# Performance work log

Measured on AMD Instinct MI355X. Metric: run time of the kernel, lower is better.

The kernel has to match this reference:

```python
import jax, jax.numpy as jnp
import numpy as np

N_NODES = 10000
N_EDGES = 640000
D_IN = 128
D_OUT = 128


def setup_inputs() -> dict:
    key = jax.random.key(0)
    ks = jax.random.split(key, 8)
    x = jax.random.normal(ks[0], (N_NODES, D_IN), dtype=jnp.float32)
    edge_index = jax.random.randint(ks[1], (2, N_EDGES), 0, N_NODES, dtype=jnp.int64)
    batch = jnp.zeros((N_NODES,), dtype=jnp.int64)
    s_in = 1.0 / np.sqrt(D_IN)
    s_out = 1.0 / np.sqrt(D_OUT)
    W_lin = jax.random.uniform(ks[2], (D_OUT, D_IN), jnp.float32, -s_in, s_in)
    b_lin = jax.random.uniform(ks[3], (D_OUT,), jnp.float32, -s_in, s_in)
    W_gate = jax.random.uniform(ks[4], (1, D_IN), jnp.float32, -s_in, s_in)
    b_gate = jax.random.uniform(ks[5], (1,), jnp.float32, -s_in, s_in)
    W_out = jax.random.uniform(ks[6], (D_OUT, D_OUT), jnp.float32, -s_out, s_out)
    b_out = jax.random.uniform(ks[7], (D_OUT,), jnp.float32, -s_out, s_out)
    return {"x": x, "edge_index": edge_index, "batch": batch,
            "W_lin": W_lin, "b_lin": b_lin, "W_gate": W_gate, "b_gate": b_gate,
            "W_out": W_out, "b_out": b_out}


def reference(x, edge_index, batch, W_lin, b_lin, W_gate, b_gate, W_out, b_out):
    row, col = edge_index[0], edge_index[1]
    n = x.shape[0]
    messages = x[col]                                      # [E, D_IN] gather
    gate = messages @ W_gate.T + b_gate                    # [E, 1]
    h = messages @ W_lin.T + b_lin                         # [E, D_OUT]
    # segment softmax over edges grouped by destination node (row)
    g = gate[:, 0]
    seg_max = jax.ops.segment_max(g, row, num_segments=n)  # -inf for empty segments (never gathered)
    e = jnp.exp(g - seg_max[row])
    denom = jax.ops.segment_sum(e, row, num_segments=n) + 1e-16
    attn = (e / denom[row])[:, None]                       # [E, 1]
    pooled = jax.ops.segment_sum(attn * h, row, num_segments=n)  # [N, D_OUT]
    return pooled @ W_out.T + b_out
```

## Files before the change

kernel.cpp:

```cpp
#include <hip/hip_runtime.h>
#include <math.h>

#define N_NODES_C 10000
#define N_EDGES_C 640000
#define DIM 128
#define NB 625
#define CAP 1344
#define CHUNK 4096
#define KPT 16
#define GATE_BLOCKS 2500
#define WC_BLOCKS 64
#define SCAT_BLOCKS ((N_EDGES_C + CHUNK - 1) / CHUNK)

__device__ __forceinline__ unsigned pack_bf16x2(float a, float b) {
    unsigned ua = __float_as_uint(a);
    unsigned ub = __float_as_uint(b);
    ua = (ua + 0x7FFFu + ((ua >> 16) & 1u)) >> 16;
    ub = (ub + 0x7FFFu + ((ub >> 16) & 1u)) >> 16;
    return ua | (ub << 16);
}
#define BF_LO(u) __uint_as_float((u) << 16)
#define BF_HI(u) __uint_as_float((u) & 0xFFFF0000u)

__global__ void prep_scatter_kernel(const float* __restrict__ x,
                                    const float* __restrict__ w_gate,
                                    const float* __restrict__ b_gate,
                                    const float* __restrict__ W_out,
                                    const float* __restrict__ W_lin,
                                    const float* __restrict__ b_lin,
                                    const int* __restrict__ row,
                                    const int* __restrict__ col,
                                    float* __restrict__ eg,
                                    unsigned* __restrict__ xh,
                                    int* __restrict__ bucket_fill,
                                    int* __restrict__ edata_b,
                                    float* __restrict__ WcT,
                                    float* __restrict__ bc,
                                    int n, int nE) {
    __shared__ int   histS[NB];
    __shared__ int   lbaseS[NB];
    __shared__ float wrow[2][DIM];
    __shared__ float red[2][DIM];
    int tid = threadIdx.x;
    int bx  = blockIdx.x;

    if (bx < SCAT_BLOCKS) {
        int sb = bx;
        for (int i = tid; i < NB; i += 256) histS[i] = 0;
        __syncthreads();

        int start = sb * CHUNK;
        int bkt[KPT], rnk[KPT], cl[KPT];
        #pragma unroll
        for (int k = 0; k < KPT; k++) {
            int e = start + k * 256 + tid;
            if (e < nE) {
                int r = row[e];
                int b = r >> 4;
                bkt[k] = b;
                cl[k]  = ((r & 15) << 16) | col[e];
                rnk[k] = atomicAdd(&histS[b], 1);
            } else { bkt[k] = -1; rnk[k] = 0; cl[k] = 0; }
        }
        __syncthreads();
        for (int i = tid; i < NB; i += 256)
            lbaseS[i] = histS[i] ? atomicAdd(&bucket_fill[i], histS[i]) : 0;
        __syncthreads();
        #pragma unroll
        for (int k = 0; k < KPT; k++) {
            if (bkt[k] >= 0) {
                int p = lbaseS[bkt[k]] + rnk[k];
                if (p < CAP)
                    edata_b[(size_t)bkt[k] * CAP + p] = cl[k];
            }
        }
    } else if (bx < SCAT_BLOCKS + WC_BLOCKS) {
        int grp = tid >> 7;
        int i   = tid & 127;
        int o   = (bx - SCAT_BLOCKS) * 2 + grp;
        wrow[grp][i] = W_out[o * DIM + i];
        __syncthreads();
        float acc = 0.f;
        #pragma unroll 8
        for (int k = 0; k < DIM; k++) acc += wrow[grp][k] * W_lin[k * DIM + i];
        WcT[i * DIM + o] = acc;
        red[grp][i] = wrow[grp][i] * b_lin[i];
        __syncthreads();
        for (int off = 64; off; off >>= 1) {
            if (i < off) red[grp][i] += red[grp][i + off];
            __syncthreads();
        }
        if (i == 0) bc[o] = red[grp][0];
    } else {
        int gid  = (bx - SCAT_BLOCKS - WC_BLOCKS) * 256 + tid;
        int wid  = gid >> 6;
        int lane = tid & 63;
        if (wid < n) {
            const float2* xr = (const float2*)(x + (size_t)wid * DIM);
            float2 a = xr[lane];
            float2 b = ((const float2*)w_gate)[lane];
            xh[(size_t)wid * 64 + lane] = pack_bf16x2(a.x, a.y);
            float v = a.x * b.x + a.y * b.y;
            #pragma unroll
            for (int off = 32; off; off >>= 1) v += __shfl_xor(v, off);
            if (lane == 0) eg[wid] = expf(v + b_gate[0]);
        }
    }
}

__global__ __launch_bounds__(512)
void bagg_kernel(const unsigned* __restrict__ xh,
                 const float* __restrict__ eg,
                 const int* __restrict__ edata_b,
                 const int* __restrict__ bucket_fill,
                 const float* __restrict__ WcT,
                 const float* __restrict__ bc,
                 const float* __restrict__ b_out,
                 float* __restrict__ out, int n) {
    __shared__ float aggT[16 * DIM];
    __shared__ float egS[N_NODES_C];
    __shared__ int  cntS[16], baseS[16], curS[16];
    __shared__ float sS[16];
    int* srt = (int*)aggT;

    int b   = blockIdx.x;
    int tid = threadIdx.x;
    int cnt = bucket_fill[b]; if (cnt > CAP) cnt = CAP;
    const int* eb = edata_b + (size_t)b * CAP;

    {
        const float4* eg4 = (const float4*)eg;
        float4* egS4 = (float4*)egS;
        #pragma unroll
        for (int k = 0; k < 5; k++) {
            int i = tid + k * 512;
            if (i < N_NODES_C / 4) egS4[i] = eg4[i];
        }
    }
    if (tid < 16) cntS[tid] = 0;
    __syncthreads();

    int rec[3];
    #pragma unroll
    for (int k = 0; k < 3; k++) {
        int j = tid + k * 512;
        rec[k] = (j < cnt) ? eb[j] : -1;
        if (rec[k] >= 0) atomicAdd(&cntS[rec[k] >> 16], 1);
    }
    __syncthreads();

    if (tid < 16) {
        int v = cntS[tid];
        int s = v;
        #pragma unroll
        for (int off = 1; off < 16; off <<= 1) {
            int t = __shfl_up(s, off);
            if (tid >= off) s += t;
        }
        baseS[tid] = s - v;
        curS[tid]  = s - v;
    }
    __syncthreads();

    #pragma unroll
    for (int k = 0; k < 3; k++) {
        if (rec[k] >= 0) {
            int p = atomicAdd(&curS[rec[k] >> 16], 1);
            srt[p] = rec[k] & 0xFFFF;
        }
    }
    __syncthreads();

    int l   = tid >> 5;
    int q   = (tid >> 4) & 1;
    int s16 = tid & 15;
    int beg = baseS[l];
    int end = beg + cntS[l];

    float a0=0.f,a1=0.f,a2=0.f,a3=0.f,a4=0.f,a5=0.f,a6=0.f,a7=0.f;
    float dl = 0.f;
    int j = beg;
    for (; j + 8 <= end; j += 8) {
        #pragma unroll
        for (int p = 0; p < 4; p++) {
            int   cc = srt[j + 2 * p + q];
            float e  = egS[cc];
            uint4 u  = ((const uint4*)(xh + (size_t)cc * 64))[s16];
            dl += e;
            a0 += e * BF_LO(u.x); a1 += e * BF_HI(u.x);
            a2 += e * BF_LO(u.y); a3 += e * BF_HI(u.y);
            a4 += e * BF_LO(u.z); a5 += e * BF_HI(u.z);
            a6 += e * BF_LO(u.w); a7 += e * BF_HI(u.w);
        }
    }
    for (; j + 2 <= end; j += 2) {
        int   cc = srt[j + q];
        float e  = egS[cc];
        uint4 u  = ((const uint4*)(xh + (size_t)cc * 64))[s16];
        dl += e;
        a0 += e * BF_LO(u.x); a1 += e * BF_HI(u.x);
        a2 += e * BF_LO(u.y); a3 += e * BF_HI(u.y);
        a4 += e * BF_LO(u.z); a5 += e * BF_HI(u.z);
        a6 += e * BF_LO(u.w); a7 += e * BF_HI(u.w);
    }
    if (j < end) {
        int   cc = srt[j];
        float e  = q ? 0.f : egS[cc];
        uint4 u  = ((const uint4*)(xh + (size_t)cc * 64))[s16];
        dl += e;
        a0 += e * BF_LO(u.x); a1 += e * BF_HI(u.x);
        a2 += e * BF_LO(u.y); a3 += e * BF_HI(u.y);
        a4 += e * BF_LO(u.z); a5 += e * BF_HI(u.z);
        a6 += e * BF_LO(u.w); a7 += e * BF_HI(u.w);
    }

    a0 += __shfl_xor(a0, 16); a1 += __shfl_xor(a1, 16);
    a2 += __shfl_xor(a2, 16); a3 += __shfl_xor(a3, 16);
    a4 += __shfl_xor(a4, 16); a5 += __shfl_xor(a5, 16);
    a6 += __shfl_xor(a6, 16); a7 += __shfl_xor(a7, 16);
    dl += __shfl_xor(dl, 16);
    float denom = dl;
    float inv   = 1.f / (denom + 1e-16f);

    __syncthreads();
    if (q == 0) {
        float4* dst = (float4*)(aggT + l * DIM + 8 * s16);
        dst[0] = make_float4(a0 * inv, a1 * inv, a2 * inv, a3 * inv);
        dst[1] = make_float4(a4 * inv, a5 * inv, a6 * inv, a7 * inv);
        if (s16 == 0) sS[l] = denom * inv;
    }
    __syncthreads();

    int grp = tid >> 7;
    int o   = tid & 127;
    int l0  = grp * 4;
    float bcv = bc[o];
    float bov = b_out[o];
    float o0 = 0.f, o1 = 0.f, o2 = 0.f, o3 = 0.f;
    const float* t0 = aggT + (l0 + 0) * DIM;
    const float* t1 = aggT + (l0 + 1) * DIM;
    const float* t2 = aggT + (l0 + 2) * DIM;
    const float* t3 = aggT + (l0 + 3) * DIM;
    #pragma unroll 4
    for (int i = 0; i < DIM; i++) {
        float w = WcT[i * DIM + o];
        o0 += w * t0[i];
        o1 += w * t1[i];
        o2 += w * t2[i];
        o3 += w * t3[i];
    }
    int nodeBase = (b << 4) + l0;
    if (nodeBase + 0 < n) out[(size_t)(nodeBase + 0) * DIM + o] = o0 + sS[l0 + 0] * bcv + bov;
    if (nodeBase + 1 < n) out[(size_t)(nodeBase + 1) * DIM + o] = o1 + sS[l0 + 1] * bcv + bov;
    if (nodeBase + 2 < n) out[(size_t)(nodeBase + 2) * DIM + o] = o2 + sS[l0 + 2] * bcv + bov;
    if (nodeBase + 3 < n) out[(size_t)(nodeBase + 3) * DIM + o] = o3 + sS[l0 + 3] * bcv + bov;
}

extern "C" void kernel_launch(void* const* d_in, const int* in_sizes, int n_in,
                              void* d_out, int out_size, void* d_ws, size_t ws_size,
                              hipStream_t stream) {
    const float* x      = (const float*)d_in[0];
    const int*   eidx   = (const int*)d_in[1];
    const float* W_lin  = (const float*)d_in[3];
    const float* b_lin  = (const float*)d_in[4];
    const float* W_gate = (const float*)d_in[5];
    const float* b_gate = (const float*)d_in[6];
    const float* W_out  = (const float*)d_in[7];
    const float* b_out  = (const float*)d_in[8];
    float* out = (float*)d_out;

    const int n  = N_NODES_C;
    const int nE = N_EDGES_C;
    const int* row = eidx;
    const int* col = eidx + nE;

    char* ws = (char*)d_ws;
    size_t off = 0;
    auto carve = [&](size_t bytes) -> char* {
        char* p = ws + off;
        off += (bytes + 255) & ~(size_t)255;
        return p;
    };
    float*    eg          = (float*)   carve((size_t)n * 4);
    unsigned* xh          = (unsigned*)carve((size_t)n * 64 * 4);
    int*      bucket_fill = (int*)     carve((size_t)NB * 4);
    int*      edata_b     = (int*)     carve((size_t)NB * CAP * 4);
    float*    WcT         = (float*)   carve((size_t)DIM * DIM * 4);
    float*    bc          = (float*)   carve((size_t)DIM * 4);

    hipMemsetAsync(bucket_fill, 0, (size_t)NB * 4, stream);
    prep_scatter_kernel<<<SCAT_BLOCKS + WC_BLOCKS + GATE_BLOCKS, 256, 0, stream>>>(
        x, W_gate, b_gate, W_out, W_lin, b_lin, row, col,
        eg, xh, bucket_fill, edata_b, WcT, bc, n, nE);
    bagg_kernel<<<NB, 512, 0, stream>>>(
        xh, eg, edata_b, bucket_fill, WcT, bc, b_out, out, n);
}
```

Before: 49.21 us.

## Halve aggregation buckets to 8 nodes and drop shared-memory gate table

Buckets now hold 8 destination nodes each (1250 buckets, CAP 704), and the aggregation kernel runs with 256 threads per block instead of 512. The kernel no longer copies the whole 40KB exp-gate array into LDS per block; it reads eg directly from global memory (L2-resident). The main gather loop is deepened to 8 outstanding row loads per thread. The aim is to cut the per-block LDS fill and LDS footprint so more blocks fit per CU, at the cost of scattered global reads for the gate values. One risk is that a bucket with more than 704 edges would be truncated, and the margin over the mean is smaller than before.

```diff
diff --git a/kernel.cpp b/kernel.cpp
--- a/kernel.cpp
+++ b/kernel.cpp
@@ -4,8 +4,8 @@
 #define N_NODES_C 10000
 #define N_EDGES_C 640000
 #define DIM 128
-#define NB 625
-#define CAP 1344
+#define NB 1250
+#define CAP 704
 #define CHUNK 4096
 #define KPT 16
 #define GATE_BLOCKS 2500
@@ -56,9 +56,9 @@
             int e = start + k * 256 + tid;
             if (e < nE) {
                 int r = row[e];
-                int b = r >> 4;
+                int b = r >> 3;
                 bkt[k] = b;
-                cl[k]  = ((r & 15) << 16) | col[e];
+                cl[k]  = ((r & 7) << 16) | col[e];
                 rnk[k] = atomicAdd(&histS[b], 1);
             } else { bkt[k] = -1; rnk[k] = 0; cl[k] = 0; }
         }
@@ -108,7 +108,7 @@
     }
 }
 
-__global__ __launch_bounds__(512)
+__global__ __launch_bounds__(256, 5)
 void bagg_kernel(const unsigned* __restrict__ xh,
                  const float* __restrict__ eg,
                  const int* __restrict__ edata_b,
@@ -117,10 +117,9 @@
                  const float* __restrict__ bc,
                  const float* __restrict__ b_out,
                  float* __restrict__ out, int n) {
-    __shared__ float aggT[16 * DIM];
-    __shared__ float egS[N_NODES_C];
-    __shared__ int  cntS[16], baseS[16], curS[16];
-    __shared__ float sS[16];
+    __shared__ float aggT[8 * DIM];
+    __shared__ int  cntS[8], baseS[8], curS[8];
+    __shared__ float sS[8];
     int* srt = (int*)aggT;
 
     int b   = blockIdx.x;
@@ -128,32 +127,23 @@
     int cnt = bucket_fill[b]; if (cnt > CAP) cnt = CAP;
     const int* eb = edata_b + (size_t)b * CAP;
 
-    {
-        const float4* eg4 = (const float4*)eg;
-        float4* egS4 = (float4*)egS;
-        #pragma unroll
-        for (int k = 0; k < 5; k++) {
-            int i = tid + k * 512;
-            if (i < N_NODES_C / 4) egS4[i] = eg4[i];
-        }
-    }
-    if (tid < 16) cntS[tid] = 0;
+    if (tid < 8) cntS[tid] = 0;
     __syncthreads();
 
     int rec[3];
     #pragma unroll
     for (int k = 0; k < 3; k++) {
-        int j = tid + k * 512;
+        int j = tid + k * 256;
         rec[k] = (j < cnt) ? eb[j] : -1;
         if (rec[k] >= 0) atomicAdd(&cntS[rec[k] >> 16], 1);
     }
     __syncthreads();
 
-    if (tid < 16) {
+    if (tid < 8) {
         int v = cntS[tid];
         int s = v;
         #pragma unroll
-        for (int off = 1; off < 16; off <<= 1) {
+        for (int off = 1; off < 8; off <<= 1) {
             int t = __shfl_up(s, off);
             if (tid >= off) s += t;
         }
@@ -180,22 +170,26 @@
     float a0=0.f,a1=0.f,a2=0.f,a3=0.f,a4=0.f,a5=0.f,a6=0.f,a7=0.f;
     float dl = 0.f;
     int j = beg;
-    for (; j + 8 <= end; j += 8) {
-        #pragma unroll
-        for (int p = 0; p < 4; p++) {
-            int   cc = srt[j + 2 * p + q];
-            float e  = egS[cc];
-            uint4 u  = ((const uint4*)(xh + (size_t)cc * 64))[s16];
-            dl += e;
-            a0 += e * BF_LO(u.x); a1 += e * BF_HI(u.x);
-            a2 += e * BF_LO(u.y); a3 += e * BF_HI(u.y);
-            a4 += e * BF_LO(u.z); a5 += e * BF_HI(u.z);
-            a6 += e * BF_LO(u.w); a7 += e * BF_HI(u.w);
+    for (; j + 16 <= end; j += 16) {
+        int cc[8]; uint4 u[8]; float e[8];
+        #pragma unroll
+        for (int p = 0; p < 8; p++) cc[p] = srt[j + 2 * p + q];
+        #pragma unroll
+        for (int p = 0; p < 8; p++) u[p] = ((const uint4*)(xh + (size_t)cc[p] * 64))[s16];
+        #pragma unroll
+        for (int p = 0; p < 8; p++) e[p] = eg[cc[p]];
+        #pragma unroll
+        for (int p = 0; p < 8; p++) {
+            dl += e[p];
+            a0 += e[p] * BF_LO(u[p].x); a1 += e[p] * BF_HI(u[p].x);
+            a2 += e[p] * BF_LO(u[p].y); a3 += e[p] * BF_HI(u[p].y);
+            a4 += e[p] * BF_LO(u[p].z); a5 += e[p] * BF_HI(u[p].z);
+            a6 += e[p] * BF_LO(u[p].w); a7 += e[p] * BF_HI(u[p].w);
         }
     }
     for (; j + 2 <= end; j += 2) {
         int   cc = srt[j + q];
-        float e  = egS[cc];
+        float e  = eg[cc];
         uint4 u  = ((const uint4*)(xh + (size_t)cc * 64))[s16];
         dl += e;
         a0 += e * BF_LO(u.x); a1 += e * BF_HI(u.x);
@@ -205,7 +199,7 @@
     }
     if (j < end) {
         int   cc = srt[j];
-        float e  = q ? 0.f : egS[cc];
+        float e  = q ? 0.f : eg[cc];
         uint4 u  = ((const uint4*)(xh + (size_t)cc * 64))[s16];
         dl += e;
         a0 += e * BF_LO(u.x); a1 += e * BF_HI(u.x);
@@ -249,7 +243,7 @@
         o2 += w * t2[i];
         o3 += w * t3[i];
     }
-    int nodeBase = (b << 4) + l0;
+    int nodeBase = (b << 3) + l0;
     if (nodeBase + 0 < n) out[(size_t)(nodeBase + 0) * DIM + o] = o0 + sS[l0 + 0] * bcv + bov;
     if (nodeBase + 1 < n) out[(size_t)(nodeBase + 1) * DIM + o] = o1 + sS[l0 + 1] * bcv + bov;
     if (nodeBase + 2 < n) out[(size_t)(nodeBase + 2) * DIM + o] = o2 + sS[l0 + 2] * bcv + bov;
@@ -292,6 +286,6 @@
     prep_scatter_kernel<<<SCAT_BLOCKS + WC_BLOCKS + GATE_BLOCKS, 256, 0, stream>>>(
         x, W_gate, b_gate, W_out, W_lin, b_lin, row, col,
         eg, xh, bucket_fill, edata_b, WcT, bc, n, nE);
-    bagg_kernel<<<NB, 512, 0, stream>>>(
+    bagg_kernel<<<NB, 256, 0, stream>>>(
         xh, eg, edata_b, bucket_fill, WcT, bc, b_out, out, n);
 }
```

Result: no change. 49.26 us (+0.1%).
